# Optimization experiments

Measured on AMD Instinct MI355X. Metric: run time of the kernel, lower is better.

## Reference

```python
import jax, jax.numpy as jnp
import numpy as np

B, LQ, LK, DQ, DKEY, DV = 8, 2048, 2048, 1024, 1024, 1024
MASK_NEG = -1e6  # d2l masked_softmax fill value


def setup_inputs() -> dict:
    key = jax.random.key(0)
    kq, kk, kv, kl, kw = jax.random.split(key, 5)
    queries = jax.random.normal(kq, (B, LQ, DQ), dtype=jnp.float32)
    keys = jax.random.normal(kk, (B, LK, DKEY), dtype=jnp.float32)
    values = jax.random.normal(kv, (B, LK, DV), dtype=jnp.float32)
    valid_lens = jax.random.randint(kl, (B,), 1, LK + 1)
    W_q = jax.random.normal(kw, (DQ, DKEY), dtype=jnp.float32) / np.sqrt(DQ)
    return {"queries": queries, "keys": keys, "values": values,
            "valid_lens": valid_lens, "W_q": W_q}


def reference(queries, keys, values, valid_lens, W_q):
    # Q projection: LazyLinear(key_dim, bias=False)
    q = jnp.einsum("bqd,dk->bqk", queries, W_q)          # [B, LQ, DKEY]
    d = q.shape[-1]
    scores = jnp.einsum("bqk,bsk->bqs", q, keys) / jnp.sqrt(jnp.asarray(d, q.dtype))
    # masked_softmax: positions >= valid_len set to -1e6 before softmax
    mask = jnp.arange(scores.shape[-1])[None, None, :] < valid_lens[:, None, None]
    scores = jnp.where(mask, scores, MASK_NEG)
    attn = jax.nn.softmax(scores, axis=-1)               # [B, LQ, LK]
    # dropout p=0.0 (eval) -> identity
    return jnp.einsum("bqs,bsv->bqv", attn, values)      # [B, LQ, DV]
```

## Files before the change

kernel.cpp:

```cpp
#include <hip/hip_runtime.h>
#include <cstdint>
#include <cstddef>

#define B_   8
#define LQ_  2048
#define LK_  2048

typedef __attribute__((ext_vector_type(8))) __bf16 bf16x8;
typedef __attribute__((ext_vector_type(4))) float f32x4;
typedef __attribute__((ext_vector_type(8))) unsigned short ushortx8;

__device__ __forceinline__ unsigned short f2bf(float f) {
  unsigned u = __builtin_bit_cast(unsigned, f);
  u = u + 0x7fffu + ((u >> 16) & 1u);
  return (unsigned short)(u >> 16);
}
__device__ __forceinline__ float bf2f(unsigned short h) {
  unsigned u = ((unsigned)h) << 16;
  return __builtin_bit_cast(float, u);
}

__device__ __forceinline__ void gld_lds16(const void* g, void* l) {
  __builtin_amdgcn_global_load_lds((__attribute__((address_space(1))) void*)(void*)g,
                                   (__attribute__((address_space(3))) void*)l, 16, 0, 0);
}

__global__ __launch_bounds__(256) void cast2_bf16_kernel(
    const float* __restrict__ in0, unsigned short* __restrict__ out0,
    const float* __restrict__ in1, unsigned short* __restrict__ out1,
    size_t half_blocks) {
  const float* in = blockIdx.x < half_blocks ? in0 : in1;
  unsigned short* out = blockIdx.x < half_blocks ? out0 : out1;
  size_t bb = blockIdx.x < half_blocks ? blockIdx.x : blockIdx.x - half_blocks;
  size_t i = (bb * 256 + threadIdx.x) * 8;
  float4 a = *(const float4*)(in + i);
  float4 b = *(const float4*)(in + i + 4);
  ushortx8 o;
  o[0] = f2bf(a.x); o[1] = f2bf(a.y); o[2] = f2bf(a.z); o[3] = f2bf(a.w);
  o[4] = f2bf(b.x); o[5] = f2bf(b.y); o[6] = f2bf(b.z); o[7] = f2bf(b.w);
  *(ushortx8*)(out + i) = o;
}

__global__ __launch_bounds__(256) void transpose_cast_kernel(
    const float* __restrict__ in, unsigned short* __restrict__ out,
    int R, int C, long in_bstride, long out_bstride) {
  __shared__ float t[32][33];
  const float* inb = in + (size_t)blockIdx.z * in_bstride;
  unsigned short* outb = out + (size_t)blockIdx.z * out_bstride;
  int c0 = blockIdx.x * 32, r0 = blockIdx.y * 32;
  int tx = threadIdx.x, ty = threadIdx.y;
#pragma unroll
  for (int k = 0; k < 4; ++k) {
    int r = ty + k * 8;
    t[r][tx] = inb[(size_t)(r0 + r) * C + c0 + tx];
  }
  __syncthreads();
#pragma unroll
  for (int k = 0; k < 4; ++k) {
    int c = ty + k * 8;
    outb[(size_t)(c0 + c) * R + r0 + tx] = f2bf(t[tx][c]);
  }
}

template <int OUTM, int SKIPN, int CLAMPK>
__global__ __launch_bounds__(256) void gemm_bt_kernel(
    const unsigned short* __restrict__ A, const unsigned short* __restrict__ B,
    void* __restrict__ Cp, int M, int N, int K,
    long a_bstride, long b_bstride, long c_bstride, float scale,
    const int* __restrict__ vlp) {
  __shared__ unsigned short lA[128 * 64];
  __shared__ unsigned short lB[128 * 64];

  const int tid = threadIdx.x;
  const int wave = tid >> 6;
  const int lane = tid & 63;
  const int lane15 = lane & 15;
  const int lhalf = lane >> 4;
  const int nt = (int)((blockIdx.x + 2 * blockIdx.z) & (gridDim.x - 1));
  const int m0 = blockIdx.y * 128;
  const int n0 = nt * 128;

  int vl = K;
  if constexpr (SKIPN || CLAMPK) vl = vlp[blockIdx.z];
  if constexpr (SKIPN) {
    if (n0 >= vl) return;
  }
  int kEnd = K;
  if constexpr (CLAMPK) {
    int ke = (vl + 63) & ~63;
    kEnd = ke < K ? ke : K;
  }

  const int wm = (wave & 1) * 64;
  const int wn = (wave >> 1) * 64;

  const unsigned short* Ab = A + (size_t)blockIdx.z * a_bstride;
  const unsigned short* Bb = B + (size_t)blockIdx.z * b_bstride;

  int sr[4], sc[4], sb[4];
#pragma unroll
  for (int j = 0; j < 4; ++j) {
    int blk = (wave * 4 + j) * 64 + lane;
    sb[j] = blk;
    sr[j] = blk >> 3;
    sc[j] = ((blk & 7) ^ ((blk >> 3) & 7)) * 8;
  }

  f32x4 acc[4][4];
#pragma unroll
  for (int i = 0; i < 4; ++i)
#pragma unroll
    for (int j = 0; j < 4; ++j)
      acc[i][j] = (f32x4){0.f, 0.f, 0.f, 0.f};

  const int rswz = lane15 & 7;

  for (int k0 = 0; k0 < kEnd; k0 += 64) {
#pragma unroll
    for (int j = 0; j < 4; ++j)
      gld_lds16(Ab + (size_t)(m0 + sr[j]) * K + (k0 + sc[j]), &lA[sb[j] * 8]);
#pragma unroll
    for (int j = 0; j < 4; ++j)
      gld_lds16(Bb + (size_t)(n0 + sr[j]) * K + (k0 + sc[j]), &lB[sb[j] * 8]);
    __syncthreads();

#pragma unroll
    for (int s = 0; s < 2; ++s) {
      const int cA = ((s * 4 + lhalf) ^ rswz) * 8;
      bf16x8 af[4], bfr[4];
#pragma unroll
      for (int i = 0; i < 4; ++i)
        af[i] = *(const bf16x8*)&lA[(wm + i * 16 + lane15) * 64 + cA];
#pragma unroll
      for (int j = 0; j < 4; ++j)
        bfr[j] = *(const bf16x8*)&lB[(wn + j * 16 + lane15) * 64 + cA];
#pragma unroll
      for (int i = 0; i < 4; ++i)
#pragma unroll
        for (int j = 0; j < 4; ++j)
          acc[i][j] = __builtin_amdgcn_mfma_f32_16x16x32_bf16(af[i], bfr[j], acc[i][j], 0, 0, 0);
    }
    __syncthreads();
  }

  const size_t boffC = (size_t)blockIdx.z * c_bstride;
#pragma unroll
  for (int i = 0; i < 4; ++i) {
    int row = m0 + wm + i * 16 + lhalf * 4;
#pragma unroll
    for (int j = 0; j < 4; ++j) {
      int col = n0 + wn + j * 16 + lane15;
#pragma unroll
      for (int r = 0; r < 4; ++r) {
        float v = acc[i][j][r];
        if constexpr (OUTM == 0) {
          ((unsigned short*)Cp + boffC)[(size_t)(row + r) * N + col] = f2bf(v);
        } else if constexpr (OUTM == 1) {
          ((unsigned short*)Cp + boffC)[(size_t)(row + r) * N + col] = f2bf(v * scale);
        } else {
          ((float*)Cp + boffC)[(size_t)(row + r) * N + col] = v;
        }
      }
    }
  }
}

__global__ __launch_bounds__(256) void softmax_kernel(unsigned short* __restrict__ scores,
                                                      const int* __restrict__ valid_lens) {
  const int row = blockIdx.x;
  const int b = row >> 11;
  const int vl = valid_lens[b];
  unsigned short* rp = scores + (size_t)row * LK_;
  const int tid = threadIdx.x;
  const int wid = tid >> 6, lane = tid & 63;
  __shared__ float sred[4];

  const int cb = tid * 8;
  ushortx8 h = *(const ushortx8*)(rp + cb);
  float x[8];
#pragma unroll
  for (int t = 0; t < 8; ++t) x[t] = bf2f(h[t]);

  float m = -3.4e38f;
#pragma unroll
  for (int t = 0; t < 8; ++t)
    if (cb + t < vl) m = fmaxf(m, x[t]);
#pragma unroll
  for (int off = 32; off >= 1; off >>= 1) m = fmaxf(m, __shfl_xor(m, off));
  if (lane == 0) sred[wid] = m;
  __syncthreads();
  m = fmaxf(fmaxf(sred[0], sred[1]), fmaxf(sred[2], sred[3]));
  __syncthreads();

  float e[8];
  float s = 0.f;
#pragma unroll
  for (int t = 0; t < 8; ++t) {
    e[t] = (cb + t < vl) ? __expf(x[t] - m) : 0.f;
    s += e[t];
  }
#pragma unroll
  for (int off = 32; off >= 1; off >>= 1) s += __shfl_xor(s, off);
  if (lane == 0) sred[wid] = s;
  __syncthreads();
  s = sred[0] + sred[1] + sred[2] + sred[3];
  float inv = 1.f / s;

  ushortx8 o;
#pragma unroll
  for (int t = 0; t < 8; ++t) o[t] = f2bf(e[t] * inv);
  *(ushortx8*)(rp + cb) = o;
}

extern "C" void kernel_launch(void* const* d_in, const int* in_sizes, int n_in,
                              void* d_out, int out_size, void* d_ws, size_t ws_size,
                              hipStream_t stream) {
  const float* queries = (const float*)d_in[0];
  const float* keys = (const float*)d_in[1];
  const float* values = (const float*)d_in[2];
  const int* valid_lens = (const int*)d_in[3];
  const float* W_q = (const float*)d_in[4];
  float* out = (float*)d_out;

  unsigned short* ws = (unsigned short*)d_ws;
  const size_t M1 = (size_t)1024 * 1024;
  unsigned short* q_bf = ws;
  unsigned short* scores = ws + 16 * M1;
  unsigned short* qry_bf = scores;
  unsigned short* valsT = ws + 48 * M1;
  unsigned short* wqT = ws + 64 * M1;
  unsigned short* keys_bf = ws + 65 * M1;

  cast2_bf16_kernel<<<dim3(16384), 256, 0, stream>>>(queries, qry_bf, keys, keys_bf, 8192);
  transpose_cast_kernel<<<dim3(32, 32, 1), dim3(32, 8), 0, stream>>>(
      W_q, wqT, 1024, 1024, 0, 0);
  transpose_cast_kernel<<<dim3(32, 64, 8), dim3(32, 8), 0, stream>>>(
      values, valsT, 2048, 1024, (long)2048 * 1024, (long)1024 * 2048);
  gemm_bt_kernel<0, 0, 0><<<dim3(8, 128, 1), 256, 0, stream>>>(
      qry_bf, wqT, q_bf, 16384, 1024, 1024, 0, 0, 0, 1.f, nullptr);
  gemm_bt_kernel<1, 1, 0><<<dim3(16, 16, 8), 256, 0, stream>>>(
      q_bf, keys_bf, scores, 2048, 2048, 1024,
      (long)2048 * 1024, (long)2048 * 1024, (long)2048 * 2048, 0.03125f, valid_lens);
  softmax_kernel<<<dim3(B_ * LQ_), 256, 0, stream>>>(scores, valid_lens);
  gemm_bt_kernel<2, 0, 1><<<dim3(8, 16, 8), 256, 0, stream>>>(
      scores, valsT, out, 2048, 1024, 2048,
      (long)2048 * 2048, (long)1024 * 2048, (long)2048 * 1024, 1.f, valid_lens);
}
```

Before: 441.9 us.

## Double-buffer GEMM LDS tiles and skip masked columns in softmax

The GEMM kernel now uses two LDS buffers, so the next K tile is loaded while the current one is multiplied, and the per-iteration barrier wait before compute goes away. Softmax rows also skip loading and storing columns beyond the 64-aligned valid length, since the final GEMM clamps K there and never reads them. LDS use per block doubles to 64KB, which may lower occupancy.

```diff
diff --git a/kernel.cpp b/kernel.cpp
--- a/kernel.cpp
+++ b/kernel.cpp
@@ -68,8 +68,8 @@
     void* __restrict__ Cp, int M, int N, int K,
     long a_bstride, long b_bstride, long c_bstride, float scale,
     const int* __restrict__ vlp) {
-  __shared__ unsigned short lA[128 * 64];
-  __shared__ unsigned short lB[128 * 64];
+  __shared__ unsigned short lA[2][128 * 64];
+  __shared__ unsigned short lB[2][128 * 64];
 
   const int tid = threadIdx.x;
   const int wave = tid >> 6;
@@ -115,14 +115,26 @@
 
   const int rswz = lane15 & 7;
 
+#pragma unroll
+  for (int j = 0; j < 4; ++j)
+    gld_lds16(Ab + (size_t)(m0 + sr[j]) * K + sc[j], &lA[0][sb[j] * 8]);
+#pragma unroll
+  for (int j = 0; j < 4; ++j)
+    gld_lds16(Bb + (size_t)(n0 + sr[j]) * K + sc[j], &lB[0][sb[j] * 8]);
+  __syncthreads();
+
+  int slot = 0;
   for (int k0 = 0; k0 < kEnd; k0 += 64) {
-#pragma unroll
-    for (int j = 0; j < 4; ++j)
-      gld_lds16(Ab + (size_t)(m0 + sr[j]) * K + (k0 + sc[j]), &lA[sb[j] * 8]);
-#pragma unroll
-    for (int j = 0; j < 4; ++j)
-      gld_lds16(Bb + (size_t)(n0 + sr[j]) * K + (k0 + sc[j]), &lB[sb[j] * 8]);
-    __syncthreads();
+    if (k0 + 64 < kEnd) {
+#pragma unroll
+      for (int j = 0; j < 4; ++j)
+        gld_lds16(Ab + (size_t)(m0 + sr[j]) * K + (k0 + 64 + sc[j]),
+                  &lA[slot ^ 1][sb[j] * 8]);
+#pragma unroll
+      for (int j = 0; j < 4; ++j)
+        gld_lds16(Bb + (size_t)(n0 + sr[j]) * K + (k0 + 64 + sc[j]),
+                  &lB[slot ^ 1][sb[j] * 8]);
+    }
 
 #pragma unroll
     for (int s = 0; s < 2; ++s) {
@@ -130,10 +142,10 @@
       bf16x8 af[4], bfr[4];
 #pragma unroll
       for (int i = 0; i < 4; ++i)
-        af[i] = *(const bf16x8*)&lA[(wm + i * 16 + lane15) * 64 + cA];
+        af[i] = *(const bf16x8*)&lA[slot][(wm + i * 16 + lane15) * 64 + cA];
 #pragma unroll
       for (int j = 0; j < 4; ++j)
-        bfr[j] = *(const bf16x8*)&lB[(wn + j * 16 + lane15) * 64 + cA];
+        bfr[j] = *(const bf16x8*)&lB[slot][(wn + j * 16 + lane15) * 64 + cA];
 #pragma unroll
       for (int i = 0; i < 4; ++i)
 #pragma unroll
@@ -141,6 +153,7 @@
           acc[i][j] = __builtin_amdgcn_mfma_f32_16x16x32_bf16(af[i], bfr[j], acc[i][j], 0, 0, 0);
     }
     __syncthreads();
+    slot ^= 1;
   }
 
   const size_t boffC = (size_t)blockIdx.z * c_bstride;
@@ -170,13 +183,16 @@
   const int row = blockIdx.x;
   const int b = row >> 11;
   const int vl = valid_lens[b];
+  const int kEnd = (vl + 63) & ~63;
   unsigned short* rp = scores + (size_t)row * LK_;
   const int tid = threadIdx.x;
   const int wid = tid >> 6, lane = tid & 63;
   __shared__ float sred[4];
 
   const int cb = tid * 8;
-  ushortx8 h = *(const ushortx8*)(rp + cb);
+  const bool act = cb < kEnd;
+  ushortx8 h = {};
+  if (act) h = *(const ushortx8*)(rp + cb);
   float x[8];
 #pragma unroll
   for (int t = 0; t < 8; ++t) x[t] = bf2f(h[t]);
@@ -206,10 +222,12 @@
   s = sred[0] + sred[1] + sred[2] + sred[3];
   float inv = 1.f / s;
 
-  ushortx8 o;
-#pragma unroll
-  for (int t = 0; t < 8; ++t) o[t] = f2bf(e[t] * inv);
-  *(ushortx8*)(rp + cb) = o;
+  if (act) {
+    ushortx8 o;
+#pragma unroll
+    for (int t = 0; t < 8; ++t) o[t] = f2bf(e[t] * inv);
+    *(ushortx8*)(rp + cb) = o;
+  }
 }
 
 extern "C" void kernel_launch(void* const* d_in, const int* in_sizes, int n_in,
```

After: 432.7 us. 2.1% less time.
